# Performance work log

Hardware: AMD Instinct MI355X
Metric: run time of the kernel (lower is better)

## Reference

```python
import jax, jax.numpy as jnp
import numpy as np

N = 50000
E = 800000
F_IN = 128
F_HID = 256   # 2 * out_channels
F_OUT = 128


def setup_inputs() -> dict:
    key = jax.random.key(0)
    ks = jax.random.split(key, 6)
    x = jax.random.normal(ks[0], (N, F_IN), dtype=jnp.float32)
    edge_index = jax.random.randint(ks[1], (2, E), 0, N, dtype=jnp.int64)
    # GCNConv params: glorot weight + zero bias (PyG default)
    s1 = (6.0 / (F_IN + F_HID)) ** 0.5
    s2 = (6.0 / (F_HID + F_OUT)) ** 0.5
    W1 = jax.random.uniform(ks[2], (F_IN, F_HID), jnp.float32, -s1, s1)
    b1 = jnp.zeros((F_HID,), jnp.float32)
    W2 = jax.random.uniform(ks[3], (F_HID, F_OUT), jnp.float32, -s2, s2)
    b2 = jnp.zeros((F_OUT,), jnp.float32)
    return {"x": x, "edge_index": edge_index, "W1": W1, "b1": b1, "W2": W2, "b2": b2}


def _gcn_conv(x, W, b, src, dst, deg_inv_sqrt, n):
    # norm per edge (self-loops already appended to src/dst)
    norm = deg_inv_sqrt[src] * deg_inv_sqrt[dst]          # [E+N]
    h = x @ W                                             # [N, F_out]
    msg = h[src] * norm[:, None]                          # [E+N, F_out] gather
    out = jax.ops.segment_sum(msg, dst, num_segments=n)   # scatter-add
    return out + b


def reference(x, edge_index, W1, b1, W2, b2):
    n = x.shape[0]
    loops = jnp.arange(n, dtype=edge_index.dtype)
    src = jnp.concatenate([edge_index[0], loops])
    dst = jnp.concatenate([edge_index[1], loops])
    # symmetric normalization with self-loops (PyG GCNConv default)
    deg = jax.ops.segment_sum(jnp.ones_like(dst, dtype=x.dtype), dst, num_segments=n)
    deg_inv_sqrt = jnp.where(deg > 0, jax.lax.rsqrt(jnp.maximum(deg, 1e-12)), 0.0)
    h = jax.nn.relu(_gcn_conv(x, W1, b1, src, dst, deg_inv_sqrt, n))
    h = jax.nn.relu(_gcn_conv(h, W2, b2, src, dst, deg_inv_sqrt, n))
    return h
```

## Files before the change

kernel.cpp:

```cpp
#include <hip/hip_runtime.h>


typedef short bf16x8 __attribute__((ext_vector_type(8)));
typedef float f32x4 __attribute__((ext_vector_type(4)));

#define LDSTRIDE 264
#define XTSTRIDE 136
#define BSHIFT 7
#define BMASK 127
#define CAPMAX 3072

__device__ inline unsigned short f2bf(float f) {
    unsigned int u = __float_as_uint(f);
    u += 0x7FFF + ((u >> 16) & 1);
    return (unsigned short)(u >> 16);
}
__device__ inline float bf2f(unsigned short h) {
    return __uint_as_float(((unsigned int)h) << 16);
}

__device__ inline void swz1(const float* W, unsigned short* Ws, int K, int N, int i) {
    int k = i / N, n = i % N;
    int KC = K >> 5;
    size_t d = ((((size_t)(n >> 4) * KC + (k >> 5)) * 64) + ((k >> 3) & 3) * 16 + (n & 15)) * 8
               + (k & 7);
    Ws[d] = f2bf(W[i]);
}
__global__ void wswz_kernel(const float* __restrict__ W1, const float* __restrict__ W2,
                            unsigned short* __restrict__ W1s, unsigned short* __restrict__ W2s,
                            int* __restrict__ ctrl) {
    int i = blockIdx.x * blockDim.x + threadIdx.x;
    if (blockIdx.x == 0) {
        for (int j = threadIdx.x; j < 512; j += 256) ctrl[j] = 0;
    }
    if (i < 32768) swz1(W1, W1s, 128, 256, i);
    else if (i < 65536) swz1(W2, W2s, 256, 128, i - 32768);
}

__global__ __launch_bounds__(256) void bin_kernel(
    const int* __restrict__ src, const int* __restrict__ dst,
    int* __restrict__ bcur, unsigned int* __restrict__ bbuf,
    int E, int cap, int nbuck) {
    __shared__ int cnt[512];
    __shared__ int base[512];
    int t = threadIdx.x;
    for (int i = t; i < nbuck; i += 256) cnt[i] = 0;
    __syncthreads();
    int e0 = blockIdx.x * 2048;
    unsigned int p_[8];
    int b_[8];
#pragma unroll
    for (int i = 0; i < 8; i++) {
        int e = e0 + i * 256 + t;
        if (e < E) {
            int s = src[e], d = dst[e];
            b_[i] = d >> BSHIFT;
            p_[i] = ((unsigned)(d & BMASK) << 24) | (unsigned)s;
            atomicAdd(&cnt[b_[i]], 1);
        } else b_[i] = -1;
    }
    __syncthreads();
    for (int b = t; b < nbuck; b += 256) {
        int c = cnt[b];
        base[b] = (c > 0) ? atomicAdd(&bcur[b], c) : 0;
    }
    __syncthreads();
    for (int i = t; i < nbuck; i += 256) cnt[i] = 0;
    __syncthreads();
#pragma unroll
    for (int i = 0; i < 8; i++) {
        if (b_[i] >= 0) {
            int b = b_[i];
            int p = base[b] + atomicAdd(&cnt[b], 1);
            if (p >= 0 && p < cap) bbuf[(size_t)b * cap + p] = p_[i];
        }
    }
}

__global__ __launch_bounds__(256) void bucket_csr_kernel(
    const int* __restrict__ bcur, const unsigned int* __restrict__ bbuf,
    const float* __restrict__ x,
    int* __restrict__ col, int* __restrict__ rowbeg, int* __restrict__ rowend,
    float* __restrict__ dinv, unsigned short* __restrict__ Xs, int N, int cap) {
    __shared__ int ldeg[128];
    __shared__ int sbeg[128];
    __shared__ int lrp[256];
    __shared__ float sdv[128];
    __shared__ int sh_col[CAPMAX];
    int b = blockIdx.x, t = threadIdx.x;
    int cnt = min(max(bcur[b], 0), cap);
    if (t < 128) ldeg[t] = 0;
    __syncthreads();
    const unsigned int* mybuf = bbuf + (size_t)b * cap;
    for (int i = t; i < cnt; i += 256)
        atomicAdd(&ldeg[mybuf[i] >> 24], 1);
    __syncthreads();
    int v = (t < 128) ? ldeg[t] : 0;
    lrp[t] = v;
    __syncthreads();
    for (int off = 1; off < 128; off <<= 1) {
        int u = (t >= off) ? lrp[t - off] : 0;
        __syncthreads();
        lrp[t] += u;
        __syncthreads();
    }
    int excl = lrp[t] - v;
    int gbase = b * cap;
    if (t < 128) {
        int r = b * 128 + t;
        float dv = rsqrtf((float)v + 1.0f);
        sdv[t] = dv;
        if (r < N) {
            rowbeg[r] = gbase + excl;
            rowend[r] = gbase + excl + v;
            dinv[r] = dv;
        }
        sbeg[t] = excl;
        ldeg[t] = excl;
    }
    __syncthreads();
    for (int i = t; i < cnt; i += 256) {
        unsigned int pr = mybuf[i];
        int p = atomicAdd(&ldeg[pr >> 24], 1);
        sh_col[p] = (int)pr;
    }
    __syncthreads();
    for (int i = t; i < cnt; i += 256) {
        int vi = sh_col[i];
        int row = ((unsigned)vi) >> 24;
        int s0 = sbeg[row];
        int s1 = ldeg[row];
        int rank = 0;
        for (int j = s0; j < s1; j++) {
            int vj = sh_col[j];
            rank += (vj < vi || (vj == vi && j < i)) ? 1 : 0;
        }
        col[gbase + s0 + rank] = vi & 0xffffff;
    }
    int rbase = b * 128;
    for (int i = t; i < 128 * 32; i += 256) {
        int rl = i >> 5;
        int gr = rbase + rl;
        if (gr >= N) break;
        float s = sdv[rl];
        float4 xv = ((const float4*)x)[(size_t)gr * 32 + (i & 31)];
        ushort4 o;
        o.x = f2bf(xv.x * s); o.y = f2bf(xv.y * s);
        o.z = f2bf(xv.z * s); o.w = f2bf(xv.w * s);
        ((ushort4*)Xs)[(size_t)gr * 32 + (i & 31)] = o;
    }
}

#define GLOAD8(Pf, col, i)                                                       \
    {                                                                            \
        ushort4 v0 = *(const ushort4*)((Pf) + (size_t)(col)[(i) + 0] * 128);     \
        ushort4 v1 = *(const ushort4*)((Pf) + (size_t)(col)[(i) + 1] * 128);     \
        ushort4 v2 = *(const ushort4*)((Pf) + (size_t)(col)[(i) + 2] * 128);     \
        ushort4 v3 = *(const ushort4*)((Pf) + (size_t)(col)[(i) + 3] * 128);     \
        ushort4 v4 = *(const ushort4*)((Pf) + (size_t)(col)[(i) + 4] * 128);     \
        ushort4 v5 = *(const ushort4*)((Pf) + (size_t)(col)[(i) + 5] * 128);     \
        ushort4 v6 = *(const ushort4*)((Pf) + (size_t)(col)[(i) + 6] * 128);     \
        ushort4 v7 = *(const ushort4*)((Pf) + (size_t)(col)[(i) + 7] * 128);     \
        ax += (bf2f(v0.x) + bf2f(v1.x)) + (bf2f(v2.x) + bf2f(v3.x))             \
            + (bf2f(v4.x) + bf2f(v5.x)) + (bf2f(v6.x) + bf2f(v7.x));            \
        ay += (bf2f(v0.y) + bf2f(v1.y)) + (bf2f(v2.y) + bf2f(v3.y))             \
            + (bf2f(v4.y) + bf2f(v5.y)) + (bf2f(v6.y) + bf2f(v7.y));            \
        az += (bf2f(v0.z) + bf2f(v1.z)) + (bf2f(v2.z) + bf2f(v3.z))             \
            + (bf2f(v4.z) + bf2f(v5.z)) + (bf2f(v6.z) + bf2f(v7.z));            \
        aw += (bf2f(v0.w) + bf2f(v1.w)) + (bf2f(v2.w) + bf2f(v3.w))             \
            + (bf2f(v4.w) + bf2f(v5.w)) + (bf2f(v6.w) + bf2f(v7.w));            \
    }

#define GTAIL8(Pf, col, i, end)                                                  \
    if ((i) < (end)) {                                                           \
        int cl = (end) - 1;                                                      \
        int e1 = (i) + 1 < (end) ? (i) + 1 : cl, e2 = (i) + 2 < (end) ? (i) + 2 : cl; \
        int e3 = (i) + 3 < (end) ? (i) + 3 : cl, e4 = (i) + 4 < (end) ? (i) + 4 : cl; \
        int e5 = (i) + 5 < (end) ? (i) + 5 : cl, e6 = (i) + 6 < (end) ? (i) + 6 : cl; \
        int e7 = (i) + 7 < (end) ? (i) + 7 : cl;                                 \
        float m1 = (i) + 1 < (end) ? 1.f : 0.f, m2 = (i) + 2 < (end) ? 1.f : 0.f; \
        float m3 = (i) + 3 < (end) ? 1.f : 0.f, m4 = (i) + 4 < (end) ? 1.f : 0.f; \
        float m5 = (i) + 5 < (end) ? 1.f : 0.f, m6 = (i) + 6 < (end) ? 1.f : 0.f; \
        float m7 = (i) + 7 < (end) ? 1.f : 0.f;                                  \
        ushort4 t0 = *(const ushort4*)((Pf) + (size_t)(col)[(i)] * 128);         \
        ushort4 t1 = *(const ushort4*)((Pf) + (size_t)(col)[e1] * 128);          \
        ushort4 t2 = *(const ushort4*)((Pf) + (size_t)(col)[e2] * 128);          \
        ushort4 t3 = *(const ushort4*)((Pf) + (size_t)(col)[e3] * 128);          \
        ushort4 t4 = *(const ushort4*)((Pf) + (size_t)(col)[e4] * 128);          \
        ushort4 t5 = *(const ushort4*)((Pf) + (size_t)(col)[e5] * 128);          \
        ushort4 t6 = *(const ushort4*)((Pf) + (size_t)(col)[e6] * 128);          \
        ushort4 t7 = *(const ushort4*)((Pf) + (size_t)(col)[e7] * 128);          \
        ax += bf2f(t0.x) + m1 * bf2f(t1.x) + m2 * bf2f(t2.x) + m3 * bf2f(t3.x)  \
            + m4 * bf2f(t4.x) + m5 * bf2f(t5.x) + m6 * bf2f(t6.x) + m7 * bf2f(t7.x); \
        ay += bf2f(t0.y) + m1 * bf2f(t1.y) + m2 * bf2f(t2.y) + m3 * bf2f(t3.y)  \
            + m4 * bf2f(t4.y) + m5 * bf2f(t5.y) + m6 * bf2f(t6.y) + m7 * bf2f(t7.y); \
        az += bf2f(t0.z) + m1 * bf2f(t1.z) + m2 * bf2f(t2.z) + m3 * bf2f(t3.z)  \
            + m4 * bf2f(t4.z) + m5 * bf2f(t5.z) + m6 * bf2f(t6.z) + m7 * bf2f(t7.z); \
        aw += bf2f(t0.w) + m1 * bf2f(t1.w) + m2 * bf2f(t2.w) + m3 * bf2f(t3.w)  \
            + m4 * bf2f(t4.w) + m5 * bf2f(t5.w) + m6 * bf2f(t6.w) + m7 * bf2f(t7.w); \
    }

__global__ __launch_bounds__(256) void gather2_kernel(
    const int* __restrict__ rowbeg, const int* __restrict__ rowend,
    const int* __restrict__ col, const unsigned short* __restrict__ P,
    const float* __restrict__ dinv, const float* __restrict__ bias,
    float* __restrict__ OF, int N) {
    int gid = blockIdx.x * blockDim.x + threadIdx.x;
    int r = gid >> 5;
    if (r >= N) return;
    int lane = gid & 31;
    const size_t off = (size_t)lane * 4;
    const unsigned short* Pf = P + off;

    ushort4 u = *(const ushort4*)(Pf + (size_t)r * 128);
    float ax = bf2f(u.x), ay = bf2f(u.y), az = bf2f(u.z), aw = bf2f(u.w);

    int beg = rowbeg[r], end = rowend[r];
    int i = beg;
    for (; i + 7 < end; i += 8) GLOAD8(Pf, col, i)
    GTAIL8(Pf, col, i, end)
    float s = dinv[r];
    float4 bb = *(const float4*)(bias + off);
    float4 o;
    o.x = fmaxf(ax * s + bb.x, 0.f);
    o.y = fmaxf(ay * s + bb.y, 0.f);
    o.z = fmaxf(az * s + bb.z, 0.f);
    o.w = fmaxf(aw * s + bb.w, 0.f);
    *(float4*)(OF + (size_t)r * 128 + off) = o;
}

__global__ __launch_bounds__(512, 4) void gemm_fused_kernel(
    const int* __restrict__ rowbeg, const int* __restrict__ rowend,
    const int* __restrict__ col, const unsigned short* __restrict__ Xs,
    const unsigned short* __restrict__ W1s, const unsigned short* __restrict__ W2s,
    const float* __restrict__ bias, const float* __restrict__ dinv,
    unsigned short* __restrict__ T, int M) {
    __shared__ unsigned short Xt[16 * XTSTRIDE];
    __shared__ unsigned short Ht[16 * LDSTRIDE];

    int t = threadIdx.x;
    int m0 = blockIdx.x * 16;
    int hw = t >> 5;
    int l  = t & 31;
    const unsigned short* Pf = Xs + (size_t)l * 4;

    {
        int r = m0 + hw;
        int rc = (r < M) ? r : (M - 1);
        ushort4 u = *(const ushort4*)(Pf + (size_t)rc * 128);
        float ax = bf2f(u.x), ay = bf2f(u.y), az = bf2f(u.z), aw = bf2f(u.w);
        int beg = rowbeg[rc], end = rowend[rc];
        int i = beg;
        for (; i + 7 < end; i += 8) GLOAD8(Pf, col, i)
        GTAIL8(Pf, col, i, end)
        float dvr = dinv[rc];
        ushort4 o;
        o.x = f2bf(ax * dvr); o.y = f2bf(ay * dvr);
        o.z = f2bf(az * dvr); o.w = f2bf(aw * dvr);
        *(ushort4*)(Xt + hw * XTSTRIDE + l * 4) = o;
    }
    __syncthreads();

    int wave = t >> 6;
    int lane = t & 63;
    int mrow = lane & 15, quad = lane >> 4;

    bf16x8 a[4];
#pragma unroll
    for (int kc = 0; kc < 4; kc++)
        a[kc] = *(const bf16x8*)(Xt + mrow * XTSTRIDE + kc * 32 + quad * 8);

    float dv[4];
#pragma unroll
    for (int i2 = 0; i2 < 4; i2++) {
        int gr = m0 + quad * 4 + i2;
        dv[i2] = dinv[gr < M ? gr : M - 1];
    }

    const bf16x8* w1v = (const bf16x8*)W1s;
    for (int nt = wave * 2; nt < wave * 2 + 2; nt++) {
        f32x4 c = {0.f, 0.f, 0.f, 0.f};
#pragma unroll
        for (int kc = 0; kc < 4; kc++) {
            bf16x8 b = w1v[(nt * 4 + kc) * 64 + lane];
            c = __builtin_amdgcn_mfma_f32_16x16x32_bf16(a[kc], b, c, 0, 0, 0);
        }
        int colc = nt * 16 + mrow;
        float bb = bias[colc];
#pragma unroll
        for (int i2 = 0; i2 < 4; i2++) {
            float v = fmaxf(c[i2] + bb, 0.f) * dv[i2];
            Ht[(quad * 4 + i2) * LDSTRIDE + colc] = f2bf(v);
        }
    }
    __syncthreads();

    bf16x8 hh[8];
    const unsigned short* hrow = Ht + mrow * LDSTRIDE + quad * 8;
#pragma unroll
    for (int kc = 0; kc < 8; kc++) hh[kc] = *(const bf16x8*)(hrow + kc * 32);
    const bf16x8* w2v = (const bf16x8*)W2s;
    {
        int nt = wave;
        f32x4 c = {0.f, 0.f, 0.f, 0.f};
#pragma unroll
        for (int kc = 0; kc < 8; kc++) {
            bf16x8 b = w2v[(nt * 8 + kc) * 64 + lane];
            c = __builtin_amdgcn_mfma_f32_16x16x32_bf16(hh[kc], b, c, 0, 0, 0);
        }
        int colc = nt * 16 + mrow;
#pragma unroll
        for (int i2 = 0; i2 < 4; i2++) {
            int gr = m0 + quad * 4 + i2;
            if (gr < M) T[(size_t)gr * 128 + colc] = f2bf(c[i2]);
        }
    }
}

extern "C" void kernel_launch(void* const* d_in, const int* in_sizes, int n_in,
                              void* d_out, int out_size, void* d_ws, size_t ws_size,
                              hipStream_t stream) {
    const float* x  = (const float*)d_in[0];
    const int* ei   = (const int*)d_in[1];
    const float* W1 = (const float*)d_in[2];
    const float* b1 = (const float*)d_in[3];
    const float* W2 = (const float*)d_in[4];
    const float* b2 = (const float*)d_in[5];
    float* out      = (float*)d_out;

    const int N = in_sizes[0] / 128;
    const int E = in_sizes[1] / 2;
    const int* src = ei;
    const int* dst = ei + E;

    const int nbuck = (N + BMASK) >> BSHIFT;
    int cap = E / nbuck + E / (4 * nbuck) + 512;
    if (cap > CAPMAX) cap = CAPMAX;

    float* ws = (float*)d_ws;
    size_t Np = ((size_t)N + 255) & ~(size_t)255;
    float*          dinv = ws;
    unsigned short* Ts   = (unsigned short*)(dinv + Np);
    unsigned short* Xs   = Ts + (size_t)N * 128;
    unsigned short* W1s  = Xs + (size_t)N * 128;
    unsigned short* W2s  = W1s + 32768;
    int* rowbeg = (int*)(W2s + 32768);
    int* rowend = rowbeg + Np;
    int* ctrl   = rowend + Np;
    int* bcur   = ctrl;
    unsigned int* bbuf = (unsigned int*)(ctrl + 512);
    int* col    = (int*)(bbuf + (size_t)nbuck * cap);

    wswz_kernel<<<256, 256, 0, stream>>>(W1, W2, W1s, W2s, ctrl);
    int nbins = (E + 2047) / 2048;
    bin_kernel<<<nbins, 256, 0, stream>>>(src, dst, bcur, bbuf, E, cap, nbuck);
    bucket_csr_kernel<<<nbuck, 256, 0, stream>>>(bcur, bbuf, x, col, rowbeg, rowend,
                                                 dinv, Xs, N, cap);

    int mtiles = (N + 15) / 16;
    gemm_fused_kernel<<<mtiles, 512, 0, stream>>>(rowbeg, rowend, col, Xs,
                                                  W1s, W2s, b1, dinv, Ts, N);

    int gth = N * 32;
    gather2_kernel<<<(gth + 255) / 256, 256, 0, stream>>>(rowbeg, rowend, col, Ts,
                                                          dinv, b2, out, N);
}
```

Measured before the change: 196.8 us.

## Widen gather loads to 16 bytes and double rows per GEMM block

The gather loops now give each lane eight bf16 features through a 16-byte load instead of four, so 16 lanes cover a row rather than 32. This halves the number of load instructions per neighbour and doubles the rows each wave handles. The fused GEMM kernel now processes 32 rows per block, with two 16-row subtiles split across its eight waves. That halves the grid and lets each W1/W2 fragment load serve more MFMAs. In exchange, fewer threads are in flight to hide gather latency, and each thread needs more registers.

```diff
diff --git a/kernel.cpp b/kernel.cpp
--- a/kernel.cpp
+++ b/kernel.cpp
@@ -2,6 +2,7 @@
 
 
 typedef short bf16x8 __attribute__((ext_vector_type(8)));
+typedef unsigned short u16x8 __attribute__((ext_vector_type(8)));
 typedef float f32x4 __attribute__((ext_vector_type(4)));
 
 #define LDSTRIDE 264
@@ -151,27 +152,22 @@
     }
 }
 
-#define GLOAD8(Pf, col, i)                                                       \
+#define QLOAD8(Pf, col, i)                                                       \
     {                                                                            \
-        ushort4 v0 = *(const ushort4*)((Pf) + (size_t)(col)[(i) + 0] * 128);     \
-        ushort4 v1 = *(const ushort4*)((Pf) + (size_t)(col)[(i) + 1] * 128);     \
-        ushort4 v2 = *(const ushort4*)((Pf) + (size_t)(col)[(i) + 2] * 128);     \
-        ushort4 v3 = *(const ushort4*)((Pf) + (size_t)(col)[(i) + 3] * 128);     \
-        ushort4 v4 = *(const ushort4*)((Pf) + (size_t)(col)[(i) + 4] * 128);     \
-        ushort4 v5 = *(const ushort4*)((Pf) + (size_t)(col)[(i) + 5] * 128);     \
-        ushort4 v6 = *(const ushort4*)((Pf) + (size_t)(col)[(i) + 6] * 128);     \
-        ushort4 v7 = *(const ushort4*)((Pf) + (size_t)(col)[(i) + 7] * 128);     \
-        ax += (bf2f(v0.x) + bf2f(v1.x)) + (bf2f(v2.x) + bf2f(v3.x))             \
-            + (bf2f(v4.x) + bf2f(v5.x)) + (bf2f(v6.x) + bf2f(v7.x));            \
-        ay += (bf2f(v0.y) + bf2f(v1.y)) + (bf2f(v2.y) + bf2f(v3.y))             \
-            + (bf2f(v4.y) + bf2f(v5.y)) + (bf2f(v6.y) + bf2f(v7.y));            \
-        az += (bf2f(v0.z) + bf2f(v1.z)) + (bf2f(v2.z) + bf2f(v3.z))             \
-            + (bf2f(v4.z) + bf2f(v5.z)) + (bf2f(v6.z) + bf2f(v7.z));            \
-        aw += (bf2f(v0.w) + bf2f(v1.w)) + (bf2f(v2.w) + bf2f(v3.w))             \
-            + (bf2f(v4.w) + bf2f(v5.w)) + (bf2f(v6.w) + bf2f(v7.w));            \
-    }
-
-#define GTAIL8(Pf, col, i, end)                                                  \
+        u16x8 v0 = *(const u16x8*)((Pf) + (size_t)(col)[(i) + 0] * 128);         \
+        u16x8 v1 = *(const u16x8*)((Pf) + (size_t)(col)[(i) + 1] * 128);         \
+        u16x8 v2 = *(const u16x8*)((Pf) + (size_t)(col)[(i) + 2] * 128);         \
+        u16x8 v3 = *(const u16x8*)((Pf) + (size_t)(col)[(i) + 3] * 128);         \
+        u16x8 v4 = *(const u16x8*)((Pf) + (size_t)(col)[(i) + 4] * 128);         \
+        u16x8 v5 = *(const u16x8*)((Pf) + (size_t)(col)[(i) + 5] * 128);         \
+        u16x8 v6 = *(const u16x8*)((Pf) + (size_t)(col)[(i) + 6] * 128);         \
+        u16x8 v7 = *(const u16x8*)((Pf) + (size_t)(col)[(i) + 7] * 128);         \
+        _Pragma("unroll") for (int j_ = 0; j_ < 8; j_++)                         \
+            acc[j_] += ((bf2f(v0[j_]) + bf2f(v1[j_])) + (bf2f(v2[j_]) + bf2f(v3[j_]))) \
+                     + ((bf2f(v4[j_]) + bf2f(v5[j_])) + (bf2f(v6[j_]) + bf2f(v7[j_]))); \
+    }
+
+#define QTAIL8(Pf, col, i, end)                                                  \
     if ((i) < (end)) {                                                           \
         int cl = (end) - 1;                                                      \
         int e1 = (i) + 1 < (end) ? (i) + 1 : cl, e2 = (i) + 2 < (end) ? (i) + 2 : cl; \
@@ -182,22 +178,18 @@
         float m3 = (i) + 3 < (end) ? 1.f : 0.f, m4 = (i) + 4 < (end) ? 1.f : 0.f; \
         float m5 = (i) + 5 < (end) ? 1.f : 0.f, m6 = (i) + 6 < (end) ? 1.f : 0.f; \
         float m7 = (i) + 7 < (end) ? 1.f : 0.f;                                  \
-        ushort4 t0 = *(const ushort4*)((Pf) + (size_t)(col)[(i)] * 128);         \
-        ushort4 t1 = *(const ushort4*)((Pf) + (size_t)(col)[e1] * 128);          \
-        ushort4 t2 = *(const ushort4*)((Pf) + (size_t)(col)[e2] * 128);          \
-        ushort4 t3 = *(const ushort4*)((Pf) + (size_t)(col)[e3] * 128);          \
-        ushort4 t4 = *(const ushort4*)((Pf) + (size_t)(col)[e4] * 128);          \
-        ushort4 t5 = *(const ushort4*)((Pf) + (size_t)(col)[e5] * 128);          \
-        ushort4 t6 = *(const ushort4*)((Pf) + (size_t)(col)[e6] * 128);          \
-        ushort4 t7 = *(const ushort4*)((Pf) + (size_t)(col)[e7] * 128);          \
-        ax += bf2f(t0.x) + m1 * bf2f(t1.x) + m2 * bf2f(t2.x) + m3 * bf2f(t3.x)  \
-            + m4 * bf2f(t4.x) + m5 * bf2f(t5.x) + m6 * bf2f(t6.x) + m7 * bf2f(t7.x); \
-        ay += bf2f(t0.y) + m1 * bf2f(t1.y) + m2 * bf2f(t2.y) + m3 * bf2f(t3.y)  \
-            + m4 * bf2f(t4.y) + m5 * bf2f(t5.y) + m6 * bf2f(t6.y) + m7 * bf2f(t7.y); \
-        az += bf2f(t0.z) + m1 * bf2f(t1.z) + m2 * bf2f(t2.z) + m3 * bf2f(t3.z)  \
-            + m4 * bf2f(t4.z) + m5 * bf2f(t5.z) + m6 * bf2f(t6.z) + m7 * bf2f(t7.z); \
-        aw += bf2f(t0.w) + m1 * bf2f(t1.w) + m2 * bf2f(t2.w) + m3 * bf2f(t3.w)  \
-            + m4 * bf2f(t4.w) + m5 * bf2f(t5.w) + m6 * bf2f(t6.w) + m7 * bf2f(t7.w); \
+        u16x8 v0 = *(const u16x8*)((Pf) + (size_t)(col)[(i)] * 128);             \
+        u16x8 v1 = *(const u16x8*)((Pf) + (size_t)(col)[e1] * 128);              \
+        u16x8 v2 = *(const u16x8*)((Pf) + (size_t)(col)[e2] * 128);              \
+        u16x8 v3 = *(const u16x8*)((Pf) + (size_t)(col)[e3] * 128);              \
+        u16x8 v4 = *(const u16x8*)((Pf) + (size_t)(col)[e4] * 128);              \
+        u16x8 v5 = *(const u16x8*)((Pf) + (size_t)(col)[e5] * 128);              \
+        u16x8 v6 = *(const u16x8*)((Pf) + (size_t)(col)[e6] * 128);              \
+        u16x8 v7 = *(const u16x8*)((Pf) + (size_t)(col)[e7] * 128);              \
+        _Pragma("unroll") for (int j_ = 0; j_ < 8; j_++)                         \
+            acc[j_] += bf2f(v0[j_]) + m1 * bf2f(v1[j_]) + m2 * bf2f(v2[j_])      \
+                     + m3 * bf2f(v3[j_]) + m4 * bf2f(v4[j_]) + m5 * bf2f(v5[j_]) \
+                     + m6 * bf2f(v6[j_]) + m7 * bf2f(v7[j_]);                    \
     }
 
 __global__ __launch_bounds__(256) void gather2_kernel(
@@ -206,27 +198,35 @@
     const float* __restrict__ dinv, const float* __restrict__ bias,
     float* __restrict__ OF, int N) {
     int gid = blockIdx.x * blockDim.x + threadIdx.x;
-    int r = gid >> 5;
+    int r = gid >> 4;
     if (r >= N) return;
-    int lane = gid & 31;
-    const size_t off = (size_t)lane * 4;
-    const unsigned short* Pf = P + off;
-
-    ushort4 u = *(const ushort4*)(Pf + (size_t)r * 128);
-    float ax = bf2f(u.x), ay = bf2f(u.y), az = bf2f(u.z), aw = bf2f(u.w);
-
+    int l = gid & 15;
+    const unsigned short* Pf = P + (size_t)l * 8;
+
+    float acc[8];
+    {
+        u16x8 u = *(const u16x8*)(Pf + (size_t)r * 128);
+#pragma unroll
+        for (int j = 0; j < 8; j++) acc[j] = bf2f(u[j]);
+    }
     int beg = rowbeg[r], end = rowend[r];
     int i = beg;
-    for (; i + 7 < end; i += 8) GLOAD8(Pf, col, i)
-    GTAIL8(Pf, col, i, end)
+    for (; i + 7 < end; i += 8) QLOAD8(Pf, col, i)
+    QTAIL8(Pf, col, i, end)
     float s = dinv[r];
-    float4 bb = *(const float4*)(bias + off);
-    float4 o;
-    o.x = fmaxf(ax * s + bb.x, 0.f);
-    o.y = fmaxf(ay * s + bb.y, 0.f);
-    o.z = fmaxf(az * s + bb.z, 0.f);
-    o.w = fmaxf(aw * s + bb.w, 0.f);
-    *(float4*)(OF + (size_t)r * 128 + off) = o;
+    float4 b0 = *(const float4*)(bias + l * 8);
+    float4 b1 = *(const float4*)(bias + l * 8 + 4);
+    float4 o0, o1;
+    o0.x = fmaxf(acc[0] * s + b0.x, 0.f);
+    o0.y = fmaxf(acc[1] * s + b0.y, 0.f);
+    o0.z = fmaxf(acc[2] * s + b0.z, 0.f);
+    o0.w = fmaxf(acc[3] * s + b0.w, 0.f);
+    o1.x = fmaxf(acc[4] * s + b1.x, 0.f);
+    o1.y = fmaxf(acc[5] * s + b1.y, 0.f);
+    o1.z = fmaxf(acc[6] * s + b1.z, 0.f);
+    o1.w = fmaxf(acc[7] * s + b1.w, 0.f);
+    *(float4*)(OF + (size_t)r * 128 + l * 8) = o0;
+    *(float4*)(OF + (size_t)r * 128 + l * 8 + 4) = o1;
 }
 
 __global__ __launch_bounds__(512, 4) void gemm_fused_kernel(
@@ -235,50 +235,56 @@
     const unsigned short* __restrict__ W1s, const unsigned short* __restrict__ W2s,
     const float* __restrict__ bias, const float* __restrict__ dinv,
     unsigned short* __restrict__ T, int M) {
-    __shared__ unsigned short Xt[16 * XTSTRIDE];
-    __shared__ unsigned short Ht[16 * LDSTRIDE];
+    __shared__ unsigned short Xt[32 * XTSTRIDE];
+    __shared__ unsigned short Ht[32 * LDSTRIDE];
 
     int t = threadIdx.x;
-    int m0 = blockIdx.x * 16;
-    int hw = t >> 5;
-    int l  = t & 31;
-    const unsigned short* Pf = Xs + (size_t)l * 4;
+    int m0 = blockIdx.x * 32;
+    int qw = t >> 4;
+    int l  = t & 15;
+    const unsigned short* Pf = Xs + (size_t)l * 8;
 
     {
-        int r = m0 + hw;
+        int r = m0 + qw;
         int rc = (r < M) ? r : (M - 1);
-        ushort4 u = *(const ushort4*)(Pf + (size_t)rc * 128);
-        float ax = bf2f(u.x), ay = bf2f(u.y), az = bf2f(u.z), aw = bf2f(u.w);
+        float acc[8];
+        {
+            u16x8 u = *(const u16x8*)(Pf + (size_t)rc * 128);
+#pragma unroll
+            for (int j = 0; j < 8; j++) acc[j] = bf2f(u[j]);
+        }
         int beg = rowbeg[rc], end = rowend[rc];
         int i = beg;
-        for (; i + 7 < end; i += 8) GLOAD8(Pf, col, i)
-        GTAIL8(Pf, col, i, end)
+        for (; i + 7 < end; i += 8) QLOAD8(Pf, col, i)
+        QTAIL8(Pf, col, i, end)
         float dvr = dinv[rc];
-        ushort4 o;
-        o.x = f2bf(ax * dvr); o.y = f2bf(ay * dvr);
-        o.z = f2bf(az * dvr); o.w = f2bf(aw * dvr);
-        *(ushort4*)(Xt + hw * XTSTRIDE + l * 4) = o;
+        u16x8 o;
+#pragma unroll
+        for (int j = 0; j < 8; j++) o[j] = f2bf(acc[j] * dvr);
+        *(u16x8*)(Xt + qw * XTSTRIDE + l * 8) = o;
     }
     __syncthreads();
 
     int wave = t >> 6;
     int lane = t & 63;
     int mrow = lane & 15, quad = lane >> 4;
+    int st = wave >> 2;
+    int wl = wave & 3;
 
     bf16x8 a[4];
 #pragma unroll
     for (int kc = 0; kc < 4; kc++)
-        a[kc] = *(const bf16x8*)(Xt + mrow * XTSTRIDE + kc * 32 + quad * 8);
+        a[kc] = *(const bf16x8*)(Xt + (st * 16 + mrow) * XTSTRIDE + kc * 32 + quad * 8);
 
     float dv[4];
 #pragma unroll
     for (int i2 = 0; i2 < 4; i2++) {
-        int gr = m0 + quad * 4 + i2;
+        int gr = m0 + st * 16 + quad * 4 + i2;
         dv[i2] = dinv[gr < M ? gr : M - 1];
     }
 
     const bf16x8* w1v = (const bf16x8*)W1s;
-    for (int nt = wave * 2; nt < wave * 2 + 2; nt++) {
+    for (int nt = wl * 4; nt < wl * 4 + 4; nt++) {
         f32x4 c = {0.f, 0.f, 0.f, 0.f};
 #pragma unroll
         for (int kc = 0; kc < 4; kc++) {
@@ -290,18 +296,17 @@
 #pragma unroll
         for (int i2 = 0; i2 < 4; i2++) {
             float v = fmaxf(c[i2] + bb, 0.f) * dv[i2];
-            Ht[(quad * 4 + i2) * LDSTRIDE + colc] = f2bf(v);
+            Ht[(st * 16 + quad * 4 + i2) * LDSTRIDE + colc] = f2bf(v);
         }
     }
     __syncthreads();
 
     bf16x8 hh[8];
-    const unsigned short* hrow = Ht + mrow * LDSTRIDE + quad * 8;
+    const unsigned short* hrow = Ht + (st * 16 + mrow) * LDSTRIDE + quad * 8;
 #pragma unroll
     for (int kc = 0; kc < 8; kc++) hh[kc] = *(const bf16x8*)(hrow + kc * 32);
     const bf16x8* w2v = (const bf16x8*)W2s;
-    {
-        int nt = wave;
+    for (int nt = wl * 2; nt < wl * 2 + 2; nt++) {
         f32x4 c = {0.f, 0.f, 0.f, 0.f};
 #pragma unroll
         for (int kc = 0; kc < 8; kc++) {
@@ -311,7 +316,7 @@
         int colc = nt * 16 + mrow;
 #pragma unroll
         for (int i2 = 0; i2 < 4; i2++) {
-            int gr = m0 + quad * 4 + i2;
+            int gr = m0 + st * 16 + quad * 4 + i2;
             if (gr < M) T[(size_t)gr * 128 + colc] = f2bf(c[i2]);
         }
     }
@@ -357,11 +362,11 @@
     bucket_csr_kernel<<<nbuck, 256, 0, stream>>>(bcur, bbuf, x, col, rowbeg, rowend,
                                                  dinv, Xs, N, cap);
 
-    int mtiles = (N + 15) / 16;
+    int mtiles = (N + 31) / 32;
     gemm_fused_kernel<<<mtiles, 512, 0, stream>>>(rowbeg, rowend, col, Xs,
                                                   W1s, W2s, b1, dinv, Ts, N);
 
-    int gth = N * 32;
+    int gth = N * 16;
     gather2_kernel<<<(gth + 255) / 256, 256, 0, stream>>>(rowbeg, rowend, col, Ts,
                                                           dinv, b2, out, N);
 }
```

Result: no change. 200.7 us (+2.0%).
